# Performance work log

Measured on AMD Instinct MI355X. Metric: run time of the kernel, lower is better.

The kernel has to match this reference:

```python
import jax, jax.numpy as jnp
import numpy as np

E = 8      # num_expert
D = 1024   # d_model
H = 2048   # expert hidden (htoh4 size)
K = 2      # top_k
N = 2048   # tokens (batch*seq)


def setup_inputs() -> dict:
    key = jax.random.key(0)
    ks = jax.random.split(key, 4)
    sc = lambda k, shape, s: jax.random.normal(k, shape, jnp.float32) * s
    return {
        "inp": jax.random.normal(ks[0], (N, D), jnp.float32),
        "Wg": sc(ks[1], (D, E), D ** -0.5),          # NaiveGate linear
        "bg": jnp.zeros((E,), jnp.float32),
        "W1": sc(ks[2], (E, D, H), D ** -0.5),        # per-expert htoh4
        "b1": jnp.zeros((E, H), jnp.float32),
        "W2": sc(ks[3], (E, H, D), H ** -0.5),        # per-expert h4toh
        "b2": jnp.zeros((E, D), jnp.float32),
    }


def reference(inp, Wg, bg, W1, b1, W2, b2):
    # NaiveGate: linear -> top_k logits -> softmax over the k selected logits
    logits = inp @ Wg + bg                              # [N, E]
    top_val, top_idx = jax.lax.top_k(logits, K)         # [N, K]
    gate_score = jax.nn.softmax(top_val, axis=-1)       # [N, K]

    # Expert grouped compute. Reference computes every expert on every token
    # (exact math, no capacity dropping); combine selects the routed ones.
    h = jax.nn.gelu(jnp.einsum('nd,edh->neh', inp, W1) + b1)   # [N, E, H]
    y = jnp.einsum('neh,ehd->ned', h, W2) + b2                 # [N, E, D]

    # Combine: equivalent to bmm(gate_score[N,1,K], x[N,K,D]) after gather.
    comb = jnp.sum(jax.nn.one_hot(top_idx, E, dtype=inp.dtype)
                   * gate_score[..., None], axis=1)            # [N, E]
    return jnp.einsum('ne,ned->nd', comb, y)                   # [N, D]
```

## Files before the change

kernel.cpp:

```cpp
#include <hip/hip_runtime.h>
#include <math.h>

#define N_TOK 2048
#define DM    1024
#define HD    2048
#define NE    8
#define RMAX  5120
#define TMAX  40

typedef short short8 __attribute__((ext_vector_type(8)));
typedef float f32x4  __attribute__((ext_vector_type(4)));

__device__ inline unsigned short f2b(float f) {
  unsigned int u = __float_as_uint(f);
  return (unsigned short)((u + 0x7FFFu + ((u >> 16) & 1u)) >> 16);
}
__device__ inline float b2f(unsigned short s) {
  return __uint_as_float(((unsigned int)s) << 16);
}
__device__ inline void gload_lds16(const void* g, void* l) {
  __builtin_amdgcn_global_load_lds(
      (const __attribute__((address_space(1))) unsigned int*)g,
      (__attribute__((address_space(3))) unsigned int*)l, 16, 0, 0);
}

__global__ void gate_kernel(const float* __restrict__ inp,
                            const float* __restrict__ Wg,
                            const float* __restrict__ bg,
                            int* __restrict__ top_idx,
                            float* __restrict__ gate_w) {
  int wave = threadIdx.x >> 6;
  int lane = threadIdx.x & 63;
  int n = blockIdx.x * 4 + wave;
  if (n >= N_TOK) return;
  float acc[NE];
#pragma unroll
  for (int e = 0; e < NE; ++e) acc[e] = 0.f;
  const float4* wg4 = reinterpret_cast<const float4*>(Wg);
#pragma unroll
  for (int i = 0; i < DM / 64; ++i) {
    int d = i * 64 + lane;
    float x = inp[n * DM + d];
    float4 w0 = wg4[d * 2 + 0];
    float4 w1 = wg4[d * 2 + 1];
    acc[0] += x * w0.x; acc[1] += x * w0.y; acc[2] += x * w0.z; acc[3] += x * w0.w;
    acc[4] += x * w1.x; acc[5] += x * w1.y; acc[6] += x * w1.z; acc[7] += x * w1.w;
  }
#pragma unroll
  for (int off = 32; off > 0; off >>= 1) {
#pragma unroll
    for (int e = 0; e < NE; ++e) acc[e] += __shfl_xor(acc[e], off);
  }
  if (lane == 0) {
    float v0 = -1e30f, v1 = -1e30f; int i0 = -1, i1 = -1;
#pragma unroll
    for (int e = 0; e < NE; ++e) {
      float v = acc[e] + bg[e];
      if (v > v0)      { v1 = v0; i1 = i0; v0 = v; i0 = e; }
      else if (v > v1) { v1 = v;  i1 = e; }
    }
    float e1 = expf(v1 - v0);
    float s  = 1.f + e1;
    top_idx[n * 2]     = i0;
    top_idx[n * 2 + 1] = i1;
    gate_w[n * 2]      = 1.f / s;
    gate_w[n * 2 + 1]  = e1 / s;
  }
}

__global__ void group_kernel(const int* __restrict__ top_idx,
                             int* __restrict__ token_of,
                             int* __restrict__ inv_g,
                             int* __restrict__ tile_expert,
                             int* __restrict__ tile_row0,
                             int* __restrict__ n_tiles) {
  __shared__ int s_wtot[4];
  int tid = threadIdx.x, lane = tid & 63, wid = tid >> 6;
  int base = 0, tiles = 0;
  for (int e = 0; e < NE; ++e) {
    int cnt = 0;
    for (int c0 = 0; c0 < N_TOK; c0 += 256) {
      int n = c0 + tid;
      int t0 = top_idx[n * 2], t1 = top_idx[n * 2 + 1];
      bool f = (t0 == e) || (t1 == e);
      int k = (t0 == e) ? 0 : 1;
      unsigned long long m = __ballot(f);
      int lp = __popcll(m & ((1ull << lane) - 1ull));
      if (lane == 0) s_wtot[wid] = __popcll(m);
      __syncthreads();
      int wbase = 0;
      for (int w = 0; w < 4; ++w) if (w < wid) wbase += s_wtot[w];
      if (f) {
        int pos = base + cnt + wbase + lp;
        token_of[pos] = n;
        inv_g[n * 2 + k] = pos;
      }
      cnt += s_wtot[0] + s_wtot[1] + s_wtot[2] + s_wtot[3];
      __syncthreads();
    }
    int padded = (cnt + 127) & ~127;
    for (int i = cnt + tid; i < padded; i += 256) token_of[base + i] = -1;
    if (tid == 0) {
      for (int t = 0; t < padded / 128; ++t) {
        tile_expert[tiles + t] = e;
        tile_row0[tiles + t]   = base + t * 128;
      }
    }
    tiles += padded / 128;
    base  += padded;
    __syncthreads();
  }
  if (tid == 0) n_tiles[0] = tiles;
}

__global__ void xcvt_kernel(const float* __restrict__ inp,
                            unsigned short* __restrict__ Xb) {
  int i = (blockIdx.x * 256 + threadIdx.x) * 8;
  float4 a = *(const float4*)(inp + i);
  float4 b = *(const float4*)(inp + i + 4);
  ushort4 pa, pb;
  pa.x = f2b(a.x); pa.y = f2b(a.y); pa.z = f2b(a.z); pa.w = f2b(a.w);
  pb.x = f2b(b.x); pb.y = f2b(b.y); pb.z = f2b(b.z); pb.w = f2b(b.w);
  *(ushort4*)(Xb + i)     = pa;
  *(ushort4*)(Xb + i + 4) = pb;
}

__global__ void wcvt_kernel(const float* __restrict__ W1,
                            const float* __restrict__ W2,
                            unsigned short* __restrict__ W1T,
                            unsigned short* __restrict__ W2T) {
  int z = blockIdx.z;
  const float* src; unsigned short* dst; int R, C;
  if (z < NE) { src = W1 + (size_t)z * DM * HD; dst = W1T + (size_t)z * DM * HD; R = DM; C = HD; }
  else        { src = W2 + (size_t)(z - NE) * HD * DM; dst = W2T + (size_t)(z - NE) * HD * DM; R = HD; C = DM; }
  int c0 = blockIdx.x * 64, r0 = blockIdx.y * 64;
  if (c0 >= C || r0 >= R) return;
  __shared__ float t[64][65];
  int tid = threadIdx.x;
#pragma unroll
  for (int p = 0; p < 16; ++p) {
    int idx = tid + p * 256;
    int r = idx >> 6, c = idx & 63;
    t[r][c] = src[(size_t)(r0 + r) * C + c0 + c];
  }
  __syncthreads();
#pragma unroll
  for (int p = 0; p < 16; ++p) {
    int idx = tid + p * 256;
    int c = idx >> 6, r = idx & 63;
    dst[(size_t)(c0 + c) * R + r0 + r] = f2b(t[r][c]);
  }
}

__global__ __launch_bounds__(256) void ffn1_mfma(
    const unsigned short* __restrict__ Xb,
    const unsigned short* __restrict__ W1T,
    const float* __restrict__ b1,
    const unsigned short* __restrict__ zbuf,
    const int* __restrict__ token_of, const int* __restrict__ tile_expert,
    const int* __restrict__ tile_row0, const int* __restrict__ n_tiles,
    unsigned short* __restrict__ Hbuf) {
  if ((int)blockIdx.x >= n_tiles[0]) return;
  int e    = tile_expert[blockIdx.x];
  int row0 = tile_row0[blockIdx.x];
  int h0   = blockIdx.y * 128;
  __shared__ __align__(16) unsigned short Asl[128][32];
  __shared__ __align__(16) unsigned short Bsl[128][32];
  int tid = threadIdx.x, lane = tid & 63;
  int wid = tid >> 6, wr = wid >> 1, wc = wid & 1;
  int l15 = lane & 15, l4 = lane >> 4;

  int tk[2];
#pragma unroll
  for (int q = 0; q < 2; ++q) tk[q] = token_of[row0 + ((tid + q * 256) >> 2)];

  f32x4 acc[4][4] = {};
  const unsigned short* W1e = W1T + (size_t)e * HD * DM;

  for (int kc = 0; kc < DM; kc += 32) {
    __syncthreads();
#pragma unroll
    for (int q = 0; q < 2; ++q) {
      int idx = tid + q * 256;
      const unsigned short* ga = (tk[q] < 0)
          ? zbuf
          : Xb + (size_t)tk[q] * DM + kc + (idx & 3) * 8;
      gload_lds16(ga, (char*)&Asl[0][0] + (size_t)idx * 16);
      const unsigned short* gb =
          W1e + (size_t)(h0 + (idx >> 2)) * DM + kc + (idx & 3) * 8;
      gload_lds16(gb, (char*)&Bsl[0][0] + (size_t)idx * 16);
    }
    __syncthreads();
    short8 a[4], b[4];
#pragma unroll
    for (int m = 0; m < 4; ++m)
      a[m] = *(const short8*)&Asl[wr * 64 + m * 16 + l15][l4 * 8];
#pragma unroll
    for (int n = 0; n < 4; ++n)
      b[n] = *(const short8*)&Bsl[wc * 64 + n * 16 + l15][l4 * 8];
#pragma unroll
    for (int m = 0; m < 4; ++m)
#pragma unroll
      for (int n = 0; n < 4; ++n)
        acc[m][n] = __builtin_amdgcn_mfma_f32_16x16x32_bf16(a[m], b[n], acc[m][n], 0, 0, 0);
  }

  float bias[4];
#pragma unroll
  for (int n = 0; n < 4; ++n) bias[n] = b1[e * HD + h0 + wc * 64 + n * 16 + l15];
#pragma unroll
  for (int m = 0; m < 4; ++m) {
#pragma unroll
    for (int n = 0; n < 4; ++n) {
      int col = h0 + wc * 64 + n * 16 + l15;
#pragma unroll
      for (int j = 0; j < 4; ++j) {
        int row = row0 + wr * 64 + m * 16 + l4 * 4 + j;
        float x = acc[m][n][j] + bias[n];
        float g = 0.5f * x * (1.f + tanhf(0.7978845608f * (x + 0.044715f * x * x * x)));
        Hbuf[(size_t)row * HD + col] = f2b(g);
      }
    }
  }
}

__global__ __launch_bounds__(256) void ffn2_mfma(
    const unsigned short* __restrict__ Hbuf,
    const unsigned short* __restrict__ W2T,
    const float* __restrict__ b2,
    const int* __restrict__ tile_expert, const int* __restrict__ tile_row0,
    const int* __restrict__ n_tiles,
    unsigned short* __restrict__ Ybuf) {
  if ((int)blockIdx.x >= n_tiles[0]) return;
  int e    = tile_expert[blockIdx.x];
  int row0 = tile_row0[blockIdx.x];
  int d0   = blockIdx.y * 128;
  __shared__ __align__(16) unsigned short Asl[128][32];
  __shared__ __align__(16) unsigned short Bsl[128][32];
  int tid = threadIdx.x, lane = tid & 63;
  int wid = tid >> 6, wr = wid >> 1, wc = wid & 1;
  int l15 = lane & 15, l4 = lane >> 4;

  f32x4 acc[4][4] = {};
  const unsigned short* W2e = W2T + (size_t)e * DM * HD;

  for (int kc = 0; kc < HD; kc += 32) {
    __syncthreads();
#pragma unroll
    for (int q = 0; q < 2; ++q) {
      int idx = tid + q * 256;
      const unsigned short* ga =
          Hbuf + (size_t)(row0 + (idx >> 2)) * HD + kc + (idx & 3) * 8;
      gload_lds16(ga, (char*)&Asl[0][0] + (size_t)idx * 16);
      const unsigned short* gb =
          W2e + (size_t)(d0 + (idx >> 2)) * HD + kc + (idx & 3) * 8;
      gload_lds16(gb, (char*)&Bsl[0][0] + (size_t)idx * 16);
    }
    __syncthreads();
    short8 a[4], b[4];
#pragma unroll
    for (int m = 0; m < 4; ++m)
      a[m] = *(const short8*)&Asl[wr * 64 + m * 16 + l15][l4 * 8];
#pragma unroll
    for (int n = 0; n < 4; ++n)
      b[n] = *(const short8*)&Bsl[wc * 64 + n * 16 + l15][l4 * 8];
#pragma unroll
    for (int m = 0; m < 4; ++m)
#pragma unroll
      for (int n = 0; n < 4; ++n)
        acc[m][n] = __builtin_amdgcn_mfma_f32_16x16x32_bf16(a[m], b[n], acc[m][n], 0, 0, 0);
  }

  float bias[4];
#pragma unroll
  for (int n = 0; n < 4; ++n) bias[n] = b2[e * DM + d0 + wc * 64 + n * 16 + l15];
#pragma unroll
  for (int m = 0; m < 4; ++m) {
#pragma unroll
    for (int n = 0; n < 4; ++n) {
      int col = d0 + wc * 64 + n * 16 + l15;
#pragma unroll
      for (int j = 0; j < 4; ++j) {
        int row = row0 + wr * 64 + m * 16 + l4 * 4 + j;
        Ybuf[(size_t)row * DM + col] = f2b(acc[m][n][j] + bias[n]);
      }
    }
  }
}

__global__ void combine_kernel(const unsigned short* __restrict__ Ybuf,
                               const int* __restrict__ inv_g,
                               const float* __restrict__ gate_w,
                               float* __restrict__ out) {
  int n = blockIdx.x;
  int r0 = inv_g[n * 2], r1 = inv_g[n * 2 + 1];
  float g0 = gate_w[n * 2], g1 = gate_w[n * 2 + 1];
  int i = threadIdx.x;
  ushort4 a = *(const ushort4*)(Ybuf + (size_t)r0 * DM + i * 4);
  ushort4 b = *(const ushort4*)(Ybuf + (size_t)r1 * DM + i * 4);
  float4 rv;
  rv.x = g0 * b2f(a.x) + g1 * b2f(b.x);
  rv.y = g0 * b2f(a.y) + g1 * b2f(b.y);
  rv.z = g0 * b2f(a.z) + g1 * b2f(b.z);
  rv.w = g0 * b2f(a.w) + g1 * b2f(b.w);
  *(float4*)(out + (size_t)n * DM + i * 4) = rv;
}

extern "C" void kernel_launch(void* const* d_in, const int* in_sizes, int n_in,
                              void* d_out, int out_size, void* d_ws, size_t ws_size,
                              hipStream_t stream) {
  const float* inp = (const float*)d_in[0];
  const float* Wg  = (const float*)d_in[1];
  const float* bg  = (const float*)d_in[2];
  const float* W1  = (const float*)d_in[3];
  const float* b1  = (const float*)d_in[4];
  const float* W2  = (const float*)d_in[5];
  const float* b2  = (const float*)d_in[6];
  float* out = (float*)d_out;

  char* ws = (char*)d_ws;
  size_t off = 0;
  auto alloc = [&](size_t bytes) {
    size_t o = off;
    off = (off + bytes + 255) & ~(size_t)255;
    return o;
  };
  int*   top_idx     = (int*)  (ws + alloc(N_TOK * 2 * sizeof(int)));
  float* gate_w      = (float*)(ws + alloc(N_TOK * 2 * sizeof(float)));
  int*   token_of    = (int*)  (ws + alloc(RMAX * sizeof(int)));
  int*   inv_g       = (int*)  (ws + alloc(N_TOK * 2 * sizeof(int)));
  int*   tile_expert = (int*)  (ws + alloc(TMAX * sizeof(int)));
  int*   tile_row0   = (int*)  (ws + alloc(TMAX * sizeof(int)));
  int*   n_tiles     = (int*)  (ws + alloc(sizeof(int)));
  unsigned short* zbuf = (unsigned short*)(ws + alloc(256));
  unsigned short* Xb   = (unsigned short*)(ws + alloc((size_t)N_TOK * DM * 2));
  unsigned short* W1T  = (unsigned short*)(ws + alloc((size_t)NE * DM * HD * 2));
  unsigned short* W2T  = (unsigned short*)(ws + alloc((size_t)NE * DM * HD * 2));
  unsigned short* Hbuf = (unsigned short*)(ws + alloc((size_t)RMAX * HD * 2));
  unsigned short* Ybuf = (unsigned short*)(ws + alloc((size_t)RMAX * DM * 2));
  (void)ws_size;

  hipMemsetAsync(zbuf, 0, 256, stream);
  gate_kernel<<<N_TOK / 4, 256, 0, stream>>>(inp, Wg, bg, top_idx, gate_w);
  group_kernel<<<1, 256, 0, stream>>>(top_idx, token_of, inv_g,
                                      tile_expert, tile_row0, n_tiles);
  xcvt_kernel<<<(N_TOK * DM) / (256 * 8), 256, 0, stream>>>(inp, Xb);
  wcvt_kernel<<<dim3(32, 32, 2 * NE), 256, 0, stream>>>(W1, W2, W1T, W2T);
  ffn1_mfma<<<dim3(TMAX, HD / 128), 256, 0, stream>>>(
      Xb, W1T, b1, zbuf, token_of, tile_expert, tile_row0, n_tiles, Hbuf);
  ffn2_mfma<<<dim3(TMAX, DM / 128), 256, 0, stream>>>(
      Hbuf, W2T, b2, tile_expert, tile_row0, n_tiles, Ybuf);
  combine_kernel<<<N_TOK, 256, 0, stream>>>(Ybuf, inv_g, gate_w, out);
}
```

Before: 159.9 us.

## Store converted expert weights in k-chunked layout with vectorized conversion

```diff
diff --git a/kernel.cpp b/kernel.cpp
--- a/kernel.cpp
+++ b/kernel.cpp
@@ -9,6 +9,7 @@
 #define TMAX  40
 
 typedef short short8 __attribute__((ext_vector_type(8)));
+typedef unsigned short u16x8 __attribute__((ext_vector_type(8)));
 typedef float f32x4  __attribute__((ext_vector_type(4)));
 
 __device__ inline unsigned short f2b(float f) {
@@ -125,36 +126,40 @@
   *(ushort4*)(Xb + i + 4) = pb;
 }
 
-__global__ void wcvt_kernel(const float* __restrict__ W1,
-                            const float* __restrict__ W2,
-                            unsigned short* __restrict__ W1T,
-                            unsigned short* __restrict__ W2T) {
+__global__ __launch_bounds__(256) void wcvt_kernel(
+    const float* __restrict__ W1, const float* __restrict__ W2,
+    unsigned short* __restrict__ W1C, unsigned short* __restrict__ W2C) {
   int z = blockIdx.z;
-  const float* src; unsigned short* dst; int R, C;
-  if (z < NE) { src = W1 + (size_t)z * DM * HD; dst = W1T + (size_t)z * DM * HD; R = DM; C = HD; }
-  else        { src = W2 + (size_t)(z - NE) * HD * DM; dst = W2T + (size_t)(z - NE) * HD * DM; R = HD; C = DM; }
-  int c0 = blockIdx.x * 64, r0 = blockIdx.y * 64;
-  if (c0 >= C || r0 >= R) return;
-  __shared__ float t[64][65];
-  int tid = threadIdx.x;
-#pragma unroll
-  for (int p = 0; p < 16; ++p) {
-    int idx = tid + p * 256;
-    int r = idx >> 6, c = idx & 63;
-    t[r][c] = src[(size_t)(r0 + r) * C + c0 + c];
+  const float* src; unsigned short* dst; int K, N;
+  if (z < NE) { src = W1 + (size_t)z * DM * HD; dst = W1C + (size_t)z * DM * HD; K = DM; N = HD; }
+  else        { src = W2 + (size_t)(z - NE) * HD * DM; dst = W2C + (size_t)(z - NE) * HD * DM; K = HD; N = DM; }
+  int n0 = blockIdx.x * 64, k0 = blockIdx.y * 64;
+  if (n0 >= N || k0 >= K) return;
+  __shared__ float s[64][68];
+  int t = threadIdx.x;
+  int q = t & 15, r0 = t >> 4;
+#pragma unroll
+  for (int p = 0; p < 4; ++p) {
+    int row = p * 16 + r0;
+    float4 v = *(const float4*)(src + (size_t)(k0 + row) * N + n0 + q * 4);
+    *(float4*)&s[row][q * 4] = v;
   }
   __syncthreads();
-#pragma unroll
-  for (int p = 0; p < 16; ++p) {
-    int idx = tid + p * 256;
-    int c = idx >> 6, r = idx & 63;
-    dst[(size_t)(c0 + c) * R + r0 + r] = f2b(t[r][c]);
+  int n = t & 63;
+  int kb0 = t >> 6;
+#pragma unroll
+  for (int p = 0; p < 2; ++p) {
+    int kb = kb0 + p * 4;
+    u16x8 o;
+#pragma unroll
+    for (int i = 0; i < 8; ++i) o[i] = f2b(s[kb * 8 + i][n]);
+    *(u16x8*)(dst + ((size_t)(k0 / 8 + kb) * N + n0 + n) * 8) = o;
   }
 }
 
 __global__ __launch_bounds__(256) void ffn1_mfma(
     const unsigned short* __restrict__ Xb,
-    const unsigned short* __restrict__ W1T,
+    const unsigned short* __restrict__ W1C,
     const float* __restrict__ b1,
     const unsigned short* __restrict__ zbuf,
     const int* __restrict__ token_of, const int* __restrict__ tile_expert,
@@ -175,7 +180,7 @@
   for (int q = 0; q < 2; ++q) tk[q] = token_of[row0 + ((tid + q * 256) >> 2)];
 
   f32x4 acc[4][4] = {};
-  const unsigned short* W1e = W1T + (size_t)e * HD * DM;
+  const unsigned short* W1e = W1C + (size_t)e * DM * HD;
 
   for (int kc = 0; kc < DM; kc += 32) {
     __syncthreads();
@@ -187,7 +192,7 @@
           : Xb + (size_t)tk[q] * DM + kc + (idx & 3) * 8;
       gload_lds16(ga, (char*)&Asl[0][0] + (size_t)idx * 16);
       const unsigned short* gb =
-          W1e + (size_t)(h0 + (idx >> 2)) * DM + kc + (idx & 3) * 8;
+          W1e + ((size_t)((kc >> 3) + (idx & 3)) * HD + h0 + (idx >> 2)) * 8;
       gload_lds16(gb, (char*)&Bsl[0][0] + (size_t)idx * 16);
     }
     __syncthreads();
@@ -226,7 +231,7 @@
 
 __global__ __launch_bounds__(256) void ffn2_mfma(
     const unsigned short* __restrict__ Hbuf,
-    const unsigned short* __restrict__ W2T,
+    const unsigned short* __restrict__ W2C,
     const float* __restrict__ b2,
     const int* __restrict__ tile_expert, const int* __restrict__ tile_row0,
     const int* __restrict__ n_tiles,
@@ -242,7 +247,7 @@
   int l15 = lane & 15, l4 = lane >> 4;
 
   f32x4 acc[4][4] = {};
-  const unsigned short* W2e = W2T + (size_t)e * DM * HD;
+  const unsigned short* W2e = W2C + (size_t)e * DM * HD;
 
   for (int kc = 0; kc < HD; kc += 32) {
     __syncthreads();
@@ -253,7 +258,7 @@
           Hbuf + (size_t)(row0 + (idx >> 2)) * HD + kc + (idx & 3) * 8;
       gload_lds16(ga, (char*)&Asl[0][0] + (size_t)idx * 16);
       const unsigned short* gb =
-          W2e + (size_t)(d0 + (idx >> 2)) * HD + kc + (idx & 3) * 8;
+          W2e + ((size_t)((kc >> 3) + (idx & 3)) * DM + d0 + (idx >> 2)) * 8;
       gload_lds16(gb, (char*)&Bsl[0][0] + (size_t)idx * 16);
     }
     __syncthreads();
@@ -334,8 +339,8 @@
   int*   n_tiles     = (int*)  (ws + alloc(sizeof(int)));
   unsigned short* zbuf = (unsigned short*)(ws + alloc(256));
   unsigned short* Xb   = (unsigned short*)(ws + alloc((size_t)N_TOK * DM * 2));
-  unsigned short* W1T  = (unsigned short*)(ws + alloc((size_t)NE * DM * HD * 2));
-  unsigned short* W2T  = (unsigned short*)(ws + alloc((size_t)NE * DM * HD * 2));
+  unsigned short* W1C  = (unsigned short*)(ws + alloc((size_t)NE * DM * HD * 2));
+  unsigned short* W2C  = (unsigned short*)(ws + alloc((size_t)NE * DM * HD * 2));
   unsigned short* Hbuf = (unsigned short*)(ws + alloc((size_t)RMAX * HD * 2));
   unsigned short* Ybuf = (unsigned short*)(ws + alloc((size_t)RMAX * DM * 2));
   (void)ws_size;
@@ -345,10 +350,10 @@
   group_kernel<<<1, 256, 0, stream>>>(top_idx, token_of, inv_g,
                                       tile_expert, tile_row0, n_tiles);
   xcvt_kernel<<<(N_TOK * DM) / (256 * 8), 256, 0, stream>>>(inp, Xb);
-  wcvt_kernel<<<dim3(32, 32, 2 * NE), 256, 0, stream>>>(W1, W2, W1T, W2T);
+  wcvt_kernel<<<dim3(32, 32, 2 * NE), 256, 0, stream>>>(W1, W2, W1C, W2C);
   ffn1_mfma<<<dim3(TMAX, HD / 128), 256, 0, stream>>>(
-      Xb, W1T, b1, zbuf, token_of, tile_expert, tile_row0, n_tiles, Hbuf);
+      Xb, W1C, b1, zbuf, token_of, tile_expert, tile_row0, n_tiles, Hbuf);
   ffn2_mfma<<<dim3(TMAX, DM / 128), 256, 0, stream>>>(
-      Hbuf, W2T, b2, tile_expert, tile_row0, n_tiles, Ybuf);
+      Hbuf, W2C, b2, tile_expert, tile_row0, n_tiles, Ybuf);
   combine_kernel<<<N_TOK, 256, 0, stream>>>(Ybuf, inv_g, gate_w, out);
 }
```

Result: slower. 165.6 us (+3.6%).
